# Kernel optimization log

Measured on AMD Instinct MI355X. Metric: run time of the kernel, lower is better.

The kernel has to match this reference:

```python
import jax, jax.numpy as jnp
import numpy as np

N_COMPANY = 16384
N_SECTOR = 64
PER_SECTOR = N_COMPANY // N_SECTOR  # 256, companies grouped contiguously by sector
WIN = 32
D_IN = 16
H_GRU = 64
H_INTRA = 64
H_INTER = 64
D_OUT = 4
E_INNER = 524288  # avg degree 32 within sectors


def setup_inputs() -> dict:
    key = jax.random.key(0)
    ks = jax.random.split(key, 20)
    s = 0.05

    daily_data_batch = jax.random.normal(ks[0], (WIN, N_COMPANY, D_IN), jnp.float32)

    rng = np.random.default_rng(0)
    dst = rng.integers(0, N_COMPANY, E_INNER)
    src = (dst // PER_SECTOR) * PER_SECTOR + rng.integers(0, PER_SECTOR, E_INNER)  # same-sector neighbors
    inner_edge = jnp.asarray(np.stack([src, dst]), jnp.int32)

    a, b = np.meshgrid(np.arange(N_SECTOR), np.arange(N_SECTOR), indexing="ij")
    oe = np.stack([a.ravel(), b.ravel()])
    oe = oe[:, oe[0] != oe[1]]  # fully-connected sector graph w/o self loops (GAT adds them)
    outer_edge = jnp.asarray(oe, jnp.int32)

    sector_ids = jnp.asarray(np.arange(N_COMPANY) // PER_SECTOR, jnp.int32)

    inp = {
        "daily_data_batch": daily_data_batch,
        "inner_edge": inner_edge,
        "outer_edge": outer_edge,
        "sector_ids": sector_ids,
        # BatchNorm1d(input_dim*window_size)
        "bn_gamma": jnp.ones((D_IN * WIN,), jnp.float32),
        "bn_beta": jnp.zeros((D_IN * WIN,), jnp.float32),
        # Graph GRU (per-node learnable initial hidden state)
        "gru_Wih": s * jax.random.normal(ks[1], (D_IN, 3 * H_GRU), jnp.float32),
        "gru_Whh": s * jax.random.normal(ks[2], (H_GRU, 3 * H_GRU), jnp.float32),
        "gru_bih": jnp.zeros((3 * H_GRU,), jnp.float32),
        "gru_bhh": jnp.zeros((3 * H_GRU,), jnp.float32),
        "gru_h0": s * jax.random.normal(ks[3], (N_COMPANY, H_GRU), jnp.float32),
        # intra-sector GATConv
        "gat1_W": s * jax.random.normal(ks[4], (H_GRU, H_INTRA), jnp.float32),
        "gat1_asrc": s * jax.random.normal(ks[5], (H_INTRA,), jnp.float32),
        "gat1_adst": s * jax.random.normal(ks[6], (H_INTRA,), jnp.float32),
        "gat1_b": jnp.zeros((H_INTRA,), jnp.float32),
        # inter-sector GATConv
        "gat2_W": s * jax.random.normal(ks[7], (H_INTRA, H_INTER), jnp.float32),
        "gat2_asrc": s * jax.random.normal(ks[8], (H_INTER,), jnp.float32),
        "gat2_adst": s * jax.random.normal(ks[9], (H_INTER,), jnp.float32),
        "gat2_b": jnp.zeros((H_INTER,), jnp.float32),
        # fusion / logit heads
        "fusion_W": s * jax.random.normal(ks[10], (H_GRU + H_INTRA + H_INTER, H_GRU), jnp.float32),
        "fusion_b": jnp.zeros((H_GRU,), jnp.float32),
        "logit_W": s * jax.random.normal(ks[11], (H_GRU, D_OUT), jnp.float32),
        "logit_b": jnp.zeros((D_OUT,), jnp.float32),
    }
    return inp


def _gat(x, edge, W, a_src, a_dst, b):
    """PyG-style single-head GATConv with default add_self_loops=True."""
    N = x.shape[0]
    h = x @ W  # [N, F]
    loops = jnp.arange(N, dtype=edge.dtype)
    src = jnp.concatenate([edge[0], loops])
    dst = jnp.concatenate([edge[1], loops])
    e = jax.nn.leaky_relu(h[src] @ a_src + h[dst] @ a_dst, 0.2)  # [E]
    # segment softmax over incoming edges per dst node
    m = jax.ops.segment_max(e, dst, num_segments=N)
    ex = jnp.exp(e - m[dst])
    denom = jax.ops.segment_sum(ex, dst, num_segments=N)
    alpha = ex / (denom[dst] + 1e-16)
    out = jax.ops.segment_sum(h[src] * alpha[:, None], dst, num_segments=N)
    return out + b


def _forward(daily_data_batch, inner_edge, outer_edge, sector_ids,
             bn_gamma, bn_beta,
             gru_Wih, gru_Whh, gru_bih, gru_bhh, gru_h0,
             gat1_W, gat1_asrc, gat1_adst, gat1_b,
             gat2_W, gat2_asrc, gat2_adst, gat2_b,
             fusion_W, fusion_b, logit_W, logit_b):
    W, N, D = daily_data_batch.shape
    # BatchNorm1d over companies (train-mode batch stats, eps=1e-5)
    xb = jnp.transpose(daily_data_batch, (1, 0, 2)).reshape(N, W * D)
    mu = xb.mean(axis=0)
    var = xb.var(axis=0)
    xb = (xb - mu) * jax.lax.rsqrt(var + 1e-5) * bn_gamma + bn_beta
    x = jnp.transpose(xb.reshape(N, W, D), (1, 0, 2))  # [W, N, D]

    # GRU over the window, per-node hidden state
    def step(h, xt):
        gi = xt @ gru_Wih + gru_bih
        gh = h @ gru_Whh + gru_bhh
        ir, iz, inn = jnp.split(gi, 3, axis=-1)
        hr, hz, hn = jnp.split(gh, 3, axis=-1)
        r = jax.nn.sigmoid(ir + hr)
        z = jax.nn.sigmoid(iz + hz)
        n = jnp.tanh(inn + r * hn)
        return (1.0 - z) * n + z * h, None

    seq_emb, _ = jax.lax.scan(step, gru_h0, x)  # [N, H_GRU]

    intra_emb = _gat(seq_emb, inner_edge, gat1_W, gat1_asrc, gat1_adst, gat1_b)  # [N, H_INTRA]

    # sector_separater + per-sector max pooling == segment_max
    sec_pool = jax.ops.segment_max(intra_emb, sector_ids, num_segments=N_SECTOR)  # [S, H_INTRA]
    sec_emb = _gat(sec_pool, outer_edge, gat2_W, gat2_asrc, gat2_adst, gat2_b)  # [S, H_INTER]
    sec_broad = sec_emb[sector_ids]  # repeat_interleave back to companies

    fusion_vec = jnp.concatenate([seq_emb, sec_broad, intra_emb], axis=-1)
    fusion_vec = jax.nn.relu(fusion_vec @ fusion_W + fusion_b)
    logits = jax.nn.softmax(fusion_vec @ logit_W + logit_b, axis=1)
    logits = jnp.cumsum(logits, axis=1)
    eps = 5e-08
    return jnp.clip(logits, eps, 1.0 - eps)


def reference(daily_data_batch, inner_edge, outer_edge, sector_ids,
              bn_gamma, bn_beta,
              gru_Wih, gru_Whh, gru_bih, gru_bhh, gru_h0,
              gat1_W, gat1_asrc, gat1_adst, gat1_b,
              gat2_W, gat2_asrc, gat2_adst, gat2_b,
              fusion_W, fusion_b, logit_W, logit_b):
    return _forward(daily_data_batch, inner_edge, outer_edge, sector_ids,
                    bn_gamma, bn_beta,
                    gru_Wih, gru_Whh, gru_bih, gru_bhh, gru_h0,
                    gat1_W, gat1_asrc, gat1_adst, gat1_b,
                    gat2_W, gat2_asrc, gat2_adst, gat2_b,
                    fusion_W, fusion_b, logit_W, logit_b)
```

## Files before the change

### kernel.cpp

```cpp
#include <hip/hip_runtime.h>

#define NC 16384
#define WIN 32
#define DI 16
#define EI 524288

typedef unsigned short u16;
typedef unsigned char u8;
typedef unsigned int u32;
typedef __attribute__((ext_vector_type(8))) short bfrag8;
typedef __attribute__((ext_vector_type(4))) float facc4;

__device__ __forceinline__ float bf2f(u16 u) { return __uint_as_float(((u32)u) << 16); }
__device__ __forceinline__ u16 f2bf(float f) {
    u32 u = __float_as_uint(f);
    u += 0x7FFFu + ((u >> 16) & 1u);
    return (u16)(u >> 16);
}
__device__ __forceinline__ float frcp(float x) { return __builtin_amdgcn_rcpf(x); }
__device__ __forceinline__ float ex2(float x) {
#if __has_builtin(__builtin_amdgcn_exp2f)
    return __builtin_amdgcn_exp2f(x);
#else
    return __expf(x * 0.69314718055994531f);
#endif
}
__device__ __forceinline__ u32 pk2bf(float a, float b) {
    u32 r;
    asm("v_cvt_pk_bf16_f32 %0, %1, %2" : "=v"(r) : "v"(a), "v"(b));
    return r;
}
__device__ __forceinline__ float lrelu(float x) { return x >= 0.0f ? x : 0.2f * x; }
__device__ __forceinline__ float loadf(const void* p, size_t i, bool f32) {
    return f32 ? ((const float*)p)[i] : bf2f(((const u16*)p)[i]);
}
__device__ __forceinline__ bool is_f32(const void* gamma) {
    return ((const u32*)gamma)[0] == 0x3F800000u;
}

#define O_WIMG  1024
#define O_BIMG  10240
#define O_BIH   16384
#define O_BHH   16576
#define O_G1W   16768
#define O_G1AS  20864
#define O_G1AD  20928
#define O_G1B   20992
#define O_G2W   21056
#define O_G2AS  25152
#define O_G2AD  25216
#define O_G2B   25280
#define O_FB    25344
#define O_LW    25408
#define O_LB    25664
#define O_FW16  25668
#define O_BNACC 31812
#define O_SEQ   40960
#define O_H1    1089536
#define O_INTRA 1613824
#define O_SPOOL 2138112
#define O_AS    2170880
#define O_AD    2187264
#define O_M     2203648

__global__ __launch_bounds__(256) void k_convert(const void* __restrict__ gamma,
                                                 const void* __restrict__ wih,
                                                 const void* __restrict__ whh,
                                                 const void* __restrict__ bih,
                                                 const void* __restrict__ bhh,
                                                 const void* __restrict__ g1w,
                                                 const void* __restrict__ g1as,
                                                 const void* __restrict__ g1ad,
                                                 const void* __restrict__ g1b,
                                                 const void* __restrict__ g2w,
                                                 const void* __restrict__ g2as,
                                                 const void* __restrict__ g2ad,
                                                 const void* __restrict__ g2b,
                                                 const void* __restrict__ fw,
                                                 const void* __restrict__ fb,
                                                 const void* __restrict__ lw,
                                                 const void* __restrict__ lb,
                                                 float* __restrict__ ws,
                                                 uint4* __restrict__ M16) {
    int gt = blockIdx.x * 256 + threadIdx.x;
    const int GS = 64 * 256;
    bool f32 = is_f32(gamma);
    const float KR = -1.4426950408889634f;
    const float KN = -2.8853900817779268f;
    u16* fw16 = (u16*)(ws + O_FW16);
    for (int i = gt; i < 12288; i += GS)
        fw16[i] = f32 ? f2bf(((const float*)fw)[i]) : ((const u16*)fw)[i];
    for (int i = gt; i < 4096; i += GS) {
        ws[O_G1W + i] = loadf(g1w, i, f32);
        ws[O_G2W + i] = loadf(g2w, i, f32);
    }
    if (gt < 64) {
        ws[O_G1AS + gt] = loadf(g1as, gt, f32);
        ws[O_G1AD + gt] = loadf(g1ad, gt, f32);
        ws[O_G1B + gt] = loadf(g1b, gt, f32);
        ws[O_G2AS + gt] = loadf(g2as, gt, f32);
        ws[O_G2AD + gt] = loadf(g2ad, gt, f32);
        ws[O_G2B + gt] = loadf(g2b, gt, f32);
        ws[O_FB + gt] = loadf(fb, gt, f32);
    }
    if (gt < 256) ws[O_LW + gt] = loadf(lw, gt, f32);
    if (gt < 4) ws[O_LB + gt] = loadf(lb, gt, f32);
    for (int i = gt; i < 1024; i += GS) ws[O_BNACC + i] = 0.f;
    const uint4 z4 = {0u, 0u, 0u, 0u};
    for (int i = gt; i < 262144; i += GS) M16[i] = z4;

    for (int i = gt; i < 9216; i += GS) {
        int trow = i / 36;
        int idx = i % 36;
        int w_ = trow >> 6, lane_ = trow & 63, li_ = lane_ & 15, q_ = lane_ >> 4;
        u16 lo, hi;
        if (idx < 24) {
            int g = idx >> 3, kc = (idx >> 2) & 1, j2 = idx & 3;
            float sc = (g < 2) ? KR : KN;
            int col = g * 64 + w_ * 16 + li_;
            int k = kc * 32 + q_ * 8 + j2 * 2;
            lo = f2bf(sc * loadf(whh, (size_t)k * 192 + col, f32));
            hi = f2bf(sc * loadf(whh, (size_t)(k + 1) * 192 + col, f32));
        } else {
            int idx2 = idx - 24;
            int g = idx2 >> 2, j2 = idx2 & 3;
            float sc = (g < 2) ? KR : KN;
            int col = g * 64 + w_ * 16 + li_;
            int k = q_ * 8 + j2 * 2;
            lo = (k < 16) ? f2bf(sc * loadf(wih, (size_t)k * 192 + col, f32)) : (u16)0;
            hi = (k + 1 < 16) ? f2bf(sc * loadf(wih, (size_t)(k + 1) * 192 + col, f32)) : (u16)0;
        }
        ((u32*)(ws + O_WIMG))[i] = (u32)lo | ((u32)hi << 16);
    }
    for (int i = gt; i < 1024; i += GS) {
        int trow = i >> 2, e = i & 3;
        int w_ = trow >> 6, lane_ = trow & 63, li_ = lane_ & 15;
        int c = w_ * 16 + li_;
        float v;
        if (e == 0) v = KR * (loadf(bih, c, f32) + loadf(bhh, c, f32));
        else if (e == 1) v = KR * (loadf(bih, 64 + c, f32) + loadf(bhh, 64 + c, f32));
        else if (e == 2) v = KN * loadf(bih, 128 + c, f32);
        else v = KN * loadf(bhh, 128 + c, f32);
        ws[O_BIMG + i] = v;
    }
}

__global__ __launch_bounds__(256) void k_prep(const void* __restrict__ daily,
                                              const void* __restrict__ gamma,
                                              float* __restrict__ bnacc,
                                              const int* __restrict__ edges,
                                              u32* __restrict__ M32) {
    __shared__ float rS[256 * 17];
    __shared__ float rQ[256 * 17];
    int bid = blockIdx.x;
    int tid = threadIdx.x;
    if (bid >= 128) {
        int g = (bid - 128) * 256 + tid;
        int4 s4 = ((const int4*)edges)[g];
        int4 d4 = ((const int4*)(edges + EI))[g];
        int ss[4] = {s4.x, s4.y, s4.z, s4.w};
        int dd[4] = {d4.x, d4.y, d4.z, d4.w};
#pragma unroll
        for (int i = 0; i < 4; i++) {
            int sl = ss[i] & 255;
            atomicAdd(&M32[dd[i] * 64 + (sl >> 2)], 1u << ((sl & 3) * 8));
        }
        return;
    }
    int w = bid >> 2, ch = bid & 3;
    bool f32 = is_f32(gamma);
    float s[16], q[16];
#pragma unroll
    for (int i = 0; i < 16; i++) { s[i] = 0.f; q[i] = 0.f; }
    for (int it = 0; it < 16; it++) {
        int c = ch * 4096 + it * 256 + tid;
        size_t base = ((size_t)w * NC + c) * DI;
        float v[16];
        if (f32) {
            const float4* p = (const float4*)((const float*)daily + base);
            float4 a = p[0], b = p[1], cc = p[2], d = p[3];
            v[0] = a.x; v[1] = a.y; v[2] = a.z; v[3] = a.w;
            v[4] = b.x; v[5] = b.y; v[6] = b.z; v[7] = b.w;
            v[8] = cc.x; v[9] = cc.y; v[10] = cc.z; v[11] = cc.w;
            v[12] = d.x; v[13] = d.y; v[14] = d.z; v[15] = d.w;
        } else {
            const uint4* p = (const uint4*)((const u16*)daily + base);
            uint4 a = p[0], b = p[1];
            u32 us[8] = {a.x, a.y, a.z, a.w, b.x, b.y, b.z, b.w};
#pragma unroll
            for (int i = 0; i < 8; i++) {
                v[2 * i] = __uint_as_float(us[i] << 16);
                v[2 * i + 1] = __uint_as_float(us[i] & 0xFFFF0000u);
            }
        }
#pragma unroll
        for (int i = 0; i < 16; i++) { s[i] += v[i]; q[i] += v[i] * v[i]; }
    }
#pragma unroll
    for (int i = 0; i < 16; i++) { rS[tid * 17 + i] = s[i]; rQ[tid * 17 + i] = q[i]; }
    __syncthreads();
    int f = tid & 15, g = tid >> 4;
    float ss = 0.f, qq = 0.f;
    for (int t = g * 16; t < g * 16 + 16; t++) { ss += rS[t * 17 + f]; qq += rQ[t * 17 + f]; }
    atomicAdd(&bnacc[w * 16 + f], ss);
    atomicAdd(&bnacc[512 + w * 16 + f], qq);
}

__global__ __launch_bounds__(256) void k_gru(const void* __restrict__ daily,
                                             const void* __restrict__ gamma,
                                             const void* __restrict__ beta,
                                             const void* __restrict__ h0_g,
                                             const float* __restrict__ ws,
                                             float* __restrict__ seq_out,
                                             u16* __restrict__ h1_out,
                                             float* __restrict__ asg,
                                             float* __restrict__ adg) {
    __shared__ __attribute__((aligned(16))) u16 sHd[2][16 * 72];
    __shared__ __attribute__((aligned(16))) u16 sXall[512 * 24];
    __shared__ float sSc[512], sSh[512];
    __shared__ float sRed[2][4][16];
    int tid = threadIdx.x;
    int w = tid >> 6, lane = tid & 63;
    int li = lane & 15, q = lane >> 4;
    int n0 = blockIdx.x * 16;
    int colw = w * 16 + li;
    bool f32 = is_f32(gamma);

    for (int f = tid; f < 512; f += 256) {
        float mu = ws[O_BNACC + f] * (1.0f / NC);
        float var = ws[O_BNACC + 512 + f] * (1.0f / NC) - mu * mu;
        float sc = loadf(gamma, f, f32) * rsqrtf(var + 1e-5f);
        sSc[f] = sc;
        sSh[f] = loadf(beta, f, f32) - mu * sc;
    }
    __syncthreads();

    for (int R = tid; R < 512; R += 256) {
        int t = R >> 4, m = R & 15;
        size_t base = ((size_t)t * NC + n0 + m) * DI;
        float xv[16];
        if (f32) {
            const float4* p = (const float4*)((const float*)daily + base);
            float4 a = p[0], b = p[1], c = p[2], d = p[3];
            xv[0] = a.x; xv[1] = a.y; xv[2] = a.z; xv[3] = a.w;
            xv[4] = b.x; xv[5] = b.y; xv[6] = b.z; xv[7] = b.w;
            xv[8] = c.x; xv[9] = c.y; xv[10] = c.z; xv[11] = c.w;
            xv[12] = d.x; xv[13] = d.y; xv[14] = d.z; xv[15] = d.w;
        } else {
            const uint4* p = (const uint4*)((const u16*)daily + base);
            uint4 a = p[0], b = p[1];
            u32 us[8] = {a.x, a.y, a.z, a.w, b.x, b.y, b.z, b.w};
#pragma unroll
            for (int i = 0; i < 8; i++) {
                xv[2 * i] = __uint_as_float(us[i] << 16);
                xv[2 * i + 1] = __uint_as_float(us[i] & 0xFFFF0000u);
            }
        }
        u32 pxu[8];
#pragma unroll
        for (int i = 0; i < 16; i += 2)
            pxu[i >> 1] = pk2bf(xv[i] * sSc[t * 16 + i] + sSh[t * 16 + i],
                                xv[i + 1] * sSc[t * 16 + i + 1] + sSh[t * 16 + i + 1]);
        *(uint4*)&sXall[R * 24] = *(const uint4*)&pxu[0];
        *(uint4*)&sXall[R * 24 + 8] = *(const uint4*)&pxu[4];
    }

    bfrag8 bh[3][2];
    bfrag8 bx[3];
    {
        const bfrag8* wf = (const bfrag8*)((const char*)(ws + O_WIMG) + (size_t)tid * 144);
        int c_ = 0;
#pragma unroll
        for (int g = 0; g < 3; g++)
#pragma unroll
            for (int kc = 0; kc < 2; kc++) bh[g][kc] = wf[c_++];
#pragma unroll
        for (int g = 0; g < 3; g++) bx[g] = wf[c_++];
    }
    float bR, bZ, bNX, bNH;
    {
        float4 b0 = ((const float4*)(ws + O_BIMG))[tid];
        bR = b0.x; bZ = b0.y; bNX = b0.z; bNH = b0.w;
    }

    float hC[4];
#pragma unroll
    for (int r = 0; r < 4; r++)
        hC[r] = loadf(h0_g, (size_t)(n0 + q * 4 + r) * 64 + colw, f32);
    {
        int hr = tid >> 4, hc = (tid & 15) * 4;
        u32 a = pk2bf(loadf(h0_g, (size_t)(n0 + hr) * 64 + hc, f32),
                      loadf(h0_g, (size_t)(n0 + hr) * 64 + hc + 1, f32));
        u32 b = pk2bf(loadf(h0_g, (size_t)(n0 + hr) * 64 + hc + 2, f32),
                      loadf(h0_g, (size_t)(n0 + hr) * 64 + hc + 3, f32));
        uint2 v2; v2.x = a; v2.y = b;
        *(uint2*)&sHd[0][hr * 72 + hc] = v2;
    }
    __syncthreads();

    bfrag8 ax = (bfrag8){0, 0, 0, 0, 0, 0, 0, 0};
    if (q < 2) ax = *(const bfrag8*)&sXall[li * 24 + q * 8];
    for (int t = 0; t < WIN; t++) {
        int p = t & 1;
        bfrag8 ah0 = *(const bfrag8*)&sHd[p][li * 72 + q * 8];
        bfrag8 ah1 = *(const bfrag8*)&sHd[p][li * 72 + 32 + q * 8];
        int tn = (t + 1) & (WIN - 1);
        bfrag8 axn = (bfrag8){0, 0, 0, 0, 0, 0, 0, 0};
        if (q < 2) axn = *(const bfrag8*)&sXall[(tn * 16 + li) * 24 + q * 8];
        facc4 aR = __builtin_amdgcn_mfma_f32_16x16x32_bf16(ax, bx[0], (facc4){bR, bR, bR, bR}, 0, 0, 0);
        facc4 aZ = __builtin_amdgcn_mfma_f32_16x16x32_bf16(ax, bx[1], (facc4){bZ, bZ, bZ, bZ}, 0, 0, 0);
        facc4 aNX = __builtin_amdgcn_mfma_f32_16x16x32_bf16(ax, bx[2], (facc4){bNX, bNX, bNX, bNX}, 0, 0, 0);
        facc4 aNH = __builtin_amdgcn_mfma_f32_16x16x32_bf16(ah0, bh[2][0], (facc4){bNH, bNH, bNH, bNH}, 0, 0, 0);
        aR = __builtin_amdgcn_mfma_f32_16x16x32_bf16(ah0, bh[0][0], aR, 0, 0, 0);
        aZ = __builtin_amdgcn_mfma_f32_16x16x32_bf16(ah0, bh[1][0], aZ, 0, 0, 0);
        aNH = __builtin_amdgcn_mfma_f32_16x16x32_bf16(ah1, bh[2][1], aNH, 0, 0, 0);
        aR = __builtin_amdgcn_mfma_f32_16x16x32_bf16(ah1, bh[0][1], aR, 0, 0, 0);
        aZ = __builtin_amdgcn_mfma_f32_16x16x32_bf16(ah1, bh[1][1], aZ, 0, 0, 0);
#pragma unroll
        for (int r = 0; r < 4; r++) {
            float gr = frcp(1.0f + ex2(aR[r]));
            float gz = frcp(1.0f + ex2(aZ[r]));
            float narg = aNX[r] + gr * aNH[r];
            float gn = 2.0f * frcp(1.0f + ex2(narg)) - 1.0f;
            hC[r] = gn + gz * (hC[r] - gn);
        }
#pragma unroll
        for (int rp = 0; rp < 4; rp += 2) {
            u32 pk = pk2bf(hC[rp], hC[rp + 1]);
            sHd[p ^ 1][(q * 4 + rp) * 72 + colw] = (u16)pk;
            sHd[p ^ 1][(q * 4 + rp + 1) * 72 + colw] = (u16)(pk >> 16);
        }
        __syncthreads();
        ax = axn;
    }

#pragma unroll
    for (int r = 0; r < 4; r++)
        seq_out[(size_t)(n0 + q * 4 + r) * 64 + colw] = hC[r];

    bfrag8 a0 = *(const bfrag8*)&sHd[0][li * 72 + q * 8];
    bfrag8 a1 = *(const bfrag8*)&sHd[0][li * 72 + 32 + q * 8];
    const facc4 zf = {0.f, 0.f, 0.f, 0.f};
    bfrag8 bg0, bg1;
#pragma unroll
    for (int j = 0; j < 8; j++) {
        bg0[j] = (short)f2bf(ws[O_G1W + (q * 8 + j) * 64 + colw]);
        bg1[j] = (short)f2bf(ws[O_G1W + (32 + q * 8 + j) * 64 + colw]);
    }
    facc4 acc = __builtin_amdgcn_mfma_f32_16x16x32_bf16(a0, bg0, zf, 0, 0, 0);
    acc = __builtin_amdgcn_mfma_f32_16x16x32_bf16(a1, bg1, acc, 0, 0, 0);
    float a1s_j = ws[O_G1AS + colw], a1d_j = ws[O_G1AD + colw];
    float pAs[4], pAd[4];
#pragma unroll
    for (int r = 0; r < 4; r++) {
        h1_out[(size_t)(n0 + q * 4 + r) * 64 + colw] = f2bf(acc[r]);
        pAs[r] = acc[r] * a1s_j;
        pAd[r] = acc[r] * a1d_j;
    }
#pragma unroll
    for (int o = 1; o < 16; o <<= 1)
#pragma unroll
        for (int r = 0; r < 4; r++) {
            pAs[r] += __shfl_xor(pAs[r], o);
            pAd[r] += __shfl_xor(pAd[r], o);
        }
    if (li == 0) {
#pragma unroll
        for (int r = 0; r < 4; r++) {
            sRed[0][w][q * 4 + r] = pAs[r];
            sRed[1][w][q * 4 + r] = pAd[r];
        }
    }
    __syncthreads();
    if (tid < 16) {
        asg[n0 + tid] = sRed[0][0][tid] + sRed[0][1][tid] + sRed[0][2][tid] + sRed[0][3][tid];
        adg[n0 + tid] = sRed[1][0][tid] + sRed[1][1][tid] + sRed[1][2][tid] + sRed[1][3][tid];
    }
}

__global__ __launch_bounds__(256) void k_gat1agg(const u16* __restrict__ h1g,
                                                 const float* __restrict__ ws,
                                                 const u8* __restrict__ M8,
                                                 const float* __restrict__ asg,
                                                 const float* __restrict__ adg,
                                                 u16* __restrict__ intra,
                                                 float* __restrict__ spool8) {
    __shared__ __attribute__((aligned(16))) u16 hT[64 * 264];
    __shared__ __attribute__((aligned(16))) u16 sP[32 * 264];
    __shared__ float sAs[256], sAd[32], sB[64], sRS[32];
    __shared__ float sRSp[8][32];
    __shared__ float wmax[4];
    int tid = threadIdx.x;
    int sector = blockIdx.x >> 3;
    int dstbase = sector * 256 + (blockIdx.x & 7) * 32;
    int sbase = sector * 256;
    {
#pragma unroll
        for (int p = 0; p < 8; p++) {
            int row = p * 32 + (tid >> 3);
            int c0 = (tid & 7) * 8;
            uint4 v = *(const uint4*)(h1g + (size_t)(sbase + row) * 64 + c0);
            u16 e[8];
            *(uint4*)e = v;
#pragma unroll
            for (int i = 0; i < 8; i++) hT[(c0 + i) * 264 + row] = e[i];
        }
    }
    sAs[tid] = asg[sbase + tid];
    if (tid < 32) sAd[tid] = adg[dstbase + tid];
    if (tid < 64) sB[tid] = ws[O_G1B + tid];
    __syncthreads();
    int lane = tid & 63, w = tid >> 6;
    int li = lane & 15, q = lane >> 4;
    {
        float a = sAs[tid];
#pragma unroll
        for (int o = 1; o < 64; o <<= 1) a = fmaxf(a, __shfl_xor(a, o));
        if (lane == 0) wmax[w] = a;
    }
    __syncthreads();
    float maxA = fmaxf(fmaxf(wmax[0], wmax[1]), fmaxf(wmax[2], wmax[3]));

    int prow = tid >> 3, pcg = tid & 7;
    {
        float adr_p = sAd[prow];
        float mrow_p = lrelu(maxA + adr_p);
        float lsum = 0.f;
        const u8* mp = M8 + (size_t)(dstbase + prow) * 256 + pcg * 32;
        uint4 mva = *(const uint4*)mp;
        uint4 mvb = *(const uint4*)(mp + 16);
        u32 wsrc[8] = {mva.x, mva.y, mva.z, mva.w, mvb.x, mvb.y, mvb.z, mvb.w};
#pragma unroll
        for (int i2 = 0; i2 < 16; i2++) {
            int i0 = 2 * i2;
            u32 mb0 = (wsrc[i0 >> 2] >> ((i0 & 3) * 8)) & 255u;
            u32 mb1 = (wsrc[i0 >> 2] >> (((i0 + 1) & 3) * 8)) & 255u;
            int c = pcg * 32 + i0;
            float e0 = lrelu(sAs[c] + adr_p);
            float e1 = lrelu(sAs[c + 1] + adr_p);
            float v0 = (float)mb0 * __expf(e0 - mrow_p);
            float v1 = (float)mb1 * __expf(e1 - mrow_p);
            u16 b0 = f2bf(v0), b1 = f2bf(v1);
            *(u32*)&sP[prow * 264 + pcg * 32 + i0] = (u32)b0 | ((u32)b1 << 16);
            lsum += bf2f(b0) + bf2f(b1);
        }
        sRSp[pcg][prow] = lsum;
    }
    __syncthreads();

    facc4 acc[2];
    acc[0] = (facc4){0.f, 0.f, 0.f, 0.f};
    acc[1] = (facc4){0.f, 0.f, 0.f, 0.f};
#pragma unroll
    for (int kc = 0; kc < 8; kc++) {
        bfrag8 bfh = *(const bfrag8*)&hT[(w * 16 + li) * 264 + kc * 32 + q * 8];
#pragma unroll
        for (int mt = 0; mt < 2; mt++) {
            bfrag8 af = *(const bfrag8*)&sP[(mt * 16 + li) * 264 + kc * 32 + q * 8];
            acc[mt] = __builtin_amdgcn_mfma_f32_16x16x32_bf16(af, bfh, acc[mt], 0, 0, 0);
        }
    }
    if (tid < 32) {
        float s = 0.f;
#pragma unroll
        for (int g = 0; g < 8; g++) s += sRSp[g][tid];
        sRS[tid] = s;
    }
    __syncthreads();

    float vmax = -1e30f;
    int colL = w * 16 + li;
#pragma unroll
    for (int mt = 0; mt < 2; mt++) {
#pragma unroll
        for (int r = 0; r < 4; r++) {
            int row = mt * 16 + q * 4 + r;
            int d = dstbase + row;
            int selfI = (blockIdx.x & 7) * 32 + row;
            float adr = sAd[row];
            float es = lrelu(sAs[selfI] + adr);
            float mrow = lrelu(maxA + adr);
            float exS = __expf(es - mrow);
            float denom = sRS[row] + exS;
            float inv = frcp(denom + 1e-16f);
            float selfh = bf2f(hT[colL * 264 + selfI]);
            float val = (acc[mt][r] + exS * selfh) * inv + sB[colL];
            intra[(size_t)d * 64 + colL] = f2bf(val);
            vmax = fmaxf(vmax, val);
        }
    }
    vmax = fmaxf(vmax, __shfl_xor(vmax, 16));
    vmax = fmaxf(vmax, __shfl_xor(vmax, 32));
    if (q == 0) spool8[(size_t)blockIdx.x * 64 + colL] = vmax;
}

__global__ __launch_bounds__(256) void k_fusion(const float* __restrict__ seq,
                                                const float* __restrict__ spool8,
                                                const u16* __restrict__ intra,
                                                const float* __restrict__ ws,
                                                const void* __restrict__ gamma,
                                                void* __restrict__ out) {
    __shared__ __attribute__((aligned(16))) union {
        struct { u16 sPmax[64 * 72]; float sH2[64 * 68]; } p0;
        struct { u16 sV[64 * 200]; float sFus[64 * 68]; } p1;
    } U;
    __shared__ float sSemb[64], sAs2[64], sAd2[64];
    __shared__ float sFB[64], sLW[256], sLB[4];
    __shared__ float red2[512];
    int tid = threadIdx.x, n0 = blockIdx.x * 64;
    int sid = blockIdx.x >> 2;
    bool f32 = is_f32(gamma);
    int lane = tid & 63, w = tid >> 6;
    int li = lane & 15, q = lane >> 4;
    int colw = w * 16 + li;

    for (int i = tid; i < 4096; i += 256) {
        int n = i >> 6, k = i & 63;
        const float* pp = &spool8[(size_t)(n * 8) * 64 + k];
        float m = pp[0];
#pragma unroll
        for (int p = 1; p < 8; p++) m = fmaxf(m, pp[p * 64]);
        U.p0.sPmax[n * 72 + k] = f2bf(m);
    }
    bfrag8 bw2[2];
#pragma unroll
    for (int kc = 0; kc < 2; kc++)
#pragma unroll
        for (int j = 0; j < 8; j++)
            bw2[kc][j] = (short)f2bf(ws[O_G2W + (kc * 32 + q * 8 + j) * 64 + colw]);
    __syncthreads();
    {
        const facc4 zf = {0.f, 0.f, 0.f, 0.f};
#pragma unroll
        for (int mt = 0; mt < 4; mt++) {
            bfrag8 af0 = *(const bfrag8*)&U.p0.sPmax[(mt * 16 + li) * 72 + q * 8];
            bfrag8 af1 = *(const bfrag8*)&U.p0.sPmax[(mt * 16 + li) * 72 + 32 + q * 8];
            facc4 a2 = __builtin_amdgcn_mfma_f32_16x16x32_bf16(af0, bw2[0], zf, 0, 0, 0);
            a2 = __builtin_amdgcn_mfma_f32_16x16x32_bf16(af1, bw2[1], a2, 0, 0, 0);
#pragma unroll
            for (int r = 0; r < 4; r++)
                U.p0.sH2[(mt * 16 + q * 4 + r) * 68 + colw] = a2[r];
        }
    }
    __syncthreads();
    {
        int n = tid >> 2, jg = tid & 3, j0 = jg * 16;
        float ps = 0.f, pd = 0.f;
#pragma unroll
        for (int i = 0; i < 16; i++) {
            float v = U.p0.sH2[n * 68 + j0 + i];
            ps += v * ws[O_G2AS + j0 + i];
            pd += v * ws[O_G2AD + j0 + i];
        }
        red2[(n * 4 + jg) * 2] = ps;
        red2[(n * 4 + jg) * 2 + 1] = pd;
    }
    __syncthreads();
    if (tid < 64) {
        float s = 0.f, dd = 0.f;
        for (int g = 0; g < 4; g++) { s += red2[(tid * 4 + g) * 2]; dd += red2[(tid * 4 + g) * 2 + 1]; }
        sAs2[tid] = s; sAd2[tid] = dd;
    }
    __syncthreads();
    if (tid < 64) {
        float e = lrelu(sAs2[tid] + sAd2[sid]);
        float m = e;
        for (int o = 32; o; o >>= 1) m = fmaxf(m, __shfl_xor(m, o));
        float ex = __expf(e - m);
        float den = ex;
        for (int o = 32; o; o >>= 1) den += __shfl_xor(den, o);
        float inv = frcp(den + 1e-16f);
        float o_ = 0.f;
        for (int l = 0; l < 64; l++) {
            float a = __shfl(ex, l);
            o_ += a * U.p0.sH2[l * 68 + tid];
        }
        sSemb[tid] = o_ * inv + ws[O_G2B + tid];
    }
    if (tid < 64) sFB[tid] = ws[O_FB + tid];
    sLW[tid] = ws[O_LW + tid];
    if (tid < 4) sLB[tid] = ws[O_LB + tid];
    __syncthreads();

    {
        int c = tid >> 2, p = tid & 3;
        u16 px[16];
        const float* rp = seq + (size_t)(n0 + c) * 64 + p * 16;
#pragma unroll
        for (int i = 0; i < 16; i += 4) {
            float4 v = *(const float4*)&rp[i];
            px[i] = f2bf(v.x); px[i + 1] = f2bf(v.y); px[i + 2] = f2bf(v.z); px[i + 3] = f2bf(v.w);
        }
        *(uint4*)&U.p1.sV[c * 200 + p * 16] = *(const uint4*)&px[0];
        *(uint4*)&U.p1.sV[c * 200 + p * 16 + 8] = *(const uint4*)&px[8];
#pragma unroll
        for (int i = 0; i < 16; i++) px[i] = f2bf(sSemb[p * 16 + i]);
        *(uint4*)&U.p1.sV[c * 200 + 64 + p * 16] = *(const uint4*)&px[0];
        *(uint4*)&U.p1.sV[c * 200 + 64 + p * 16 + 8] = *(const uint4*)&px[8];
        const u16* ip = intra + (size_t)(n0 + c) * 64 + p * 16;
        *(uint4*)&U.p1.sV[c * 200 + 128 + p * 16] = *(const uint4*)ip;
        *(uint4*)&U.p1.sV[c * 200 + 128 + p * 16 + 8] = *(const uint4*)(ip + 8);
    }
    const u16* fw16g = (const u16*)(ws + O_FW16);
    bfrag8 bwf[6];
#pragma unroll
    for (int kc = 0; kc < 6; kc++)
#pragma unroll
        for (int j = 0; j < 8; j++)
            bwf[kc][j] = (short)fw16g[(kc * 32 + q * 8 + j) * 64 + colw];
    __syncthreads();

    facc4 acc[4];
#pragma unroll
    for (int mt = 0; mt < 4; mt++) acc[mt] = (facc4){0.f, 0.f, 0.f, 0.f};
#pragma unroll
    for (int kc = 0; kc < 6; kc++) {
#pragma unroll
        for (int mt = 0; mt < 4; mt++) {
            bfrag8 av = *(const bfrag8*)&U.p1.sV[(mt * 16 + li) * 200 + kc * 32 + q * 8];
            acc[mt] = __builtin_amdgcn_mfma_f32_16x16x32_bf16(av, bwf[kc], acc[mt], 0, 0, 0);
        }
    }
    float fb = sFB[colw];
#pragma unroll
    for (int mt = 0; mt < 4; mt++)
#pragma unroll
        for (int r = 0; r < 4; r++) {
            float v = fmaxf(acc[mt][r] + fb, 0.f);
            U.p1.sFus[(mt * 16 + q * 4 + r) * 68 + colw] = v;
        }
    __syncthreads();

    if (tid < 64) {
        float l[4] = {sLB[0], sLB[1], sLB[2], sLB[3]};
        for (int j = 0; j < 64; j++) {
            float v = U.p1.sFus[tid * 68 + j];
            l[0] += v * sLW[j * 4 + 0];
            l[1] += v * sLW[j * 4 + 1];
            l[2] += v * sLW[j * 4 + 2];
            l[3] += v * sLW[j * 4 + 3];
        }
        float m = fmaxf(fmaxf(l[0], l[1]), fmaxf(l[2], l[3]));
        float e0 = __expf(l[0] - m), e1 = __expf(l[1] - m), e2 = __expf(l[2] - m), e3 = __expf(l[3] - m);
        float is = frcp(e0 + e1 + e2 + e3);
        float c0 = e0 * is;
        float c1 = c0 + e1 * is;
        float c2 = c1 + e2 * is;
        float c3 = c2 + e3 * is;
        const float lo = 5e-8f, hi = 1.0f - 5e-8f;
        c0 = fminf(fmaxf(c0, lo), hi);
        c1 = fminf(fmaxf(c1, lo), hi);
        c2 = fminf(fmaxf(c2, lo), hi);
        c3 = fminf(fmaxf(c3, lo), hi);
        size_t ob = (size_t)(n0 + tid) * 4;
        if (f32) {
            *(float4*)&((float*)out)[ob] = make_float4(c0, c1, c2, c3);
        } else {
            *(ushort4*)&((u16*)out)[ob] = make_ushort4(f2bf(c0), f2bf(c1), f2bf(c2), f2bf(c3));
        }
    }
}

extern "C" void kernel_launch(void* const* d_in, const int* in_sizes, int n_in,
                              void* d_out, int out_size, void* d_ws, size_t ws_size,
                              hipStream_t stream) {
    const void* daily = d_in[0];
    const int* inner = (const int*)d_in[1];
    const void* gamma = d_in[4];
    const void* beta = d_in[5];
    const void* wih = d_in[6];
    const void* whh = d_in[7];
    const void* bih = d_in[8];
    const void* bhh = d_in[9];
    const void* h0 = d_in[10];
    const void* g1w = d_in[11];
    const void* g1as = d_in[12];
    const void* g1ad = d_in[13];
    const void* g1b = d_in[14];
    const void* g2w = d_in[15];
    const void* g2as = d_in[16];
    const void* g2ad = d_in[17];
    const void* g2b = d_in[18];
    const void* fw = d_in[19];
    const void* fb = d_in[20];
    const void* lw = d_in[21];
    const void* lb = d_in[22];

    float* ws = (float*)d_ws;
    u16* h1g = (u16*)(ws + O_H1);
    u16* intra = (u16*)(ws + O_INTRA);
    u8* M8 = (u8*)(ws + O_M);

    k_convert<<<64, 256, 0, stream>>>(gamma, wih, whh, bih, bhh, g1w, g1as, g1ad, g1b,
                                      g2w, g2as, g2ad, g2b, fw, fb, lw, lb, ws, (uint4*)M8);
    k_prep<<<640, 256, 0, stream>>>(daily, gamma, ws + O_BNACC, inner, (u32*)M8);
    k_gru<<<1024, 256, 0, stream>>>(daily, gamma, beta, h0, ws, ws + O_SEQ, h1g, ws + O_AS, ws + O_AD);
    k_gat1agg<<<512, 256, 0, stream>>>(h1g, ws, M8, ws + O_AS, ws + O_AD, intra, ws + O_SPOOL);
    k_fusion<<<256, 256, 0, stream>>>(ws + O_SEQ, ws + O_SPOOL, intra, ws, gamma, d_out);
}
```

Measured before the change: 212.7 us.

## Split sector GAT into single-block kernel and parallelize fusion logits head

The sector-level GAT (pooling, projection, attention) was previously recomputed redundantly in each of the 256 fusion blocks. It now runs once in a new single-block kernel that writes all 64 sector embeddings into the workspace, reusing the spool buffer. The fusion kernel just loads its sector's embedding. The final logit/softmax/cumsum stage now uses all 256 threads (four per company, with shuffles) instead of 64. The cost is an extra kernel launch and a serial one-block kernel on the critical path.

```diff
diff --git a/kernel.cpp b/kernel.cpp
--- a/kernel.cpp
+++ b/kernel.cpp
@@ -494,25 +494,16 @@
     if (q == 0) spool8[(size_t)blockIdx.x * 64 + colL] = vmax;
 }
 
-__global__ __launch_bounds__(256) void k_fusion(const float* __restrict__ seq,
-                                                const float* __restrict__ spool8,
-                                                const u16* __restrict__ intra,
-                                                const float* __restrict__ ws,
-                                                const void* __restrict__ gamma,
-                                                void* __restrict__ out) {
-    __shared__ __attribute__((aligned(16))) union {
-        struct { u16 sPmax[64 * 72]; float sH2[64 * 68]; } p0;
-        struct { u16 sV[64 * 200]; float sFus[64 * 68]; } p1;
-    } U;
-    __shared__ float sSemb[64], sAs2[64], sAd2[64];
-    __shared__ float sFB[64], sLW[256], sLB[4];
+__global__ __launch_bounds__(256) void k_gat2(float* __restrict__ ws) {
+    __shared__ __attribute__((aligned(16))) u16 sPmax[64 * 72];
+    __shared__ float sH2[64 * 68];
+    __shared__ float sAs2[64], sAd2[64];
     __shared__ float red2[512];
-    int tid = threadIdx.x, n0 = blockIdx.x * 64;
-    int sid = blockIdx.x >> 2;
-    bool f32 = is_f32(gamma);
+    int tid = threadIdx.x;
     int lane = tid & 63, w = tid >> 6;
     int li = lane & 15, q = lane >> 4;
     int colw = w * 16 + li;
+    const float* spool8 = ws + O_SPOOL;
 
     for (int i = tid; i < 4096; i += 256) {
         int n = i >> 6, k = i & 63;
@@ -520,7 +511,7 @@
         float m = pp[0];
 #pragma unroll
         for (int p = 1; p < 8; p++) m = fmaxf(m, pp[p * 64]);
-        U.p0.sPmax[n * 72 + k] = f2bf(m);
+        sPmax[n * 72 + k] = f2bf(m);
     }
     bfrag8 bw2[2];
 #pragma unroll
@@ -533,13 +524,13 @@
         const facc4 zf = {0.f, 0.f, 0.f, 0.f};
 #pragma unroll
         for (int mt = 0; mt < 4; mt++) {
-            bfrag8 af0 = *(const bfrag8*)&U.p0.sPmax[(mt * 16 + li) * 72 + q * 8];
-            bfrag8 af1 = *(const bfrag8*)&U.p0.sPmax[(mt * 16 + li) * 72 + 32 + q * 8];
+            bfrag8 af0 = *(const bfrag8*)&sPmax[(mt * 16 + li) * 72 + q * 8];
+            bfrag8 af1 = *(const bfrag8*)&sPmax[(mt * 16 + li) * 72 + 32 + q * 8];
             facc4 a2 = __builtin_amdgcn_mfma_f32_16x16x32_bf16(af0, bw2[0], zf, 0, 0, 0);
             a2 = __builtin_amdgcn_mfma_f32_16x16x32_bf16(af1, bw2[1], a2, 0, 0, 0);
 #pragma unroll
             for (int r = 0; r < 4; r++)
-                U.p0.sH2[(mt * 16 + q * 4 + r) * 68 + colw] = a2[r];
+                sH2[(mt * 16 + q * 4 + r) * 68 + colw] = a2[r];
         }
     }
     __syncthreads();
@@ -548,7 +539,7 @@
         float ps = 0.f, pd = 0.f;
 #pragma unroll
         for (int i = 0; i < 16; i++) {
-            float v = U.p0.sH2[n * 68 + j0 + i];
+            float v = sH2[n * 68 + j0 + i];
             ps += v * ws[O_G2AS + j0 + i];
             pd += v * ws[O_G2AD + j0 + i];
         }
@@ -562,8 +553,12 @@
         sAs2[tid] = s; sAd2[tid] = dd;
     }
     __syncthreads();
-    if (tid < 64) {
-        float e = lrelu(sAs2[tid] + sAd2[sid]);
+    float as_l = sAs2[lane];
+    float* semb = ws + O_SPOOL;
+    float g2b_l = ws[O_G2B + lane];
+    for (int d0 = 0; d0 < 16; d0++) {
+        int dst = w * 16 + d0;
+        float e = lrelu(as_l + sAd2[dst]);
         float m = e;
         for (int o = 32; o; o >>= 1) m = fmaxf(m, __shfl_xor(m, o));
         float ex = __expf(e - m);
@@ -573,11 +568,32 @@
         float o_ = 0.f;
         for (int l = 0; l < 64; l++) {
             float a = __shfl(ex, l);
-            o_ += a * U.p0.sH2[l * 68 + tid];
-        }
-        sSemb[tid] = o_ * inv + ws[O_G2B + tid];
-    }
-    if (tid < 64) sFB[tid] = ws[O_FB + tid];
+            o_ += a * sH2[l * 68 + lane];
+        }
+        semb[dst * 64 + lane] = o_ * inv + g2b_l;
+    }
+}
+
+__global__ __launch_bounds__(256) void k_fusion(const float* __restrict__ seq,
+                                                const float* __restrict__ semb,
+                                                const u16* __restrict__ intra,
+                                                const float* __restrict__ ws,
+                                                const void* __restrict__ gamma,
+                                                void* __restrict__ out) {
+    __shared__ __attribute__((aligned(16))) u16 sV[64 * 200];
+    __shared__ float sFus[64 * 68];
+    __shared__ float sSemb[64], sFB[64], sLW[256], sLB[4];
+    int tid = threadIdx.x, n0 = blockIdx.x * 64;
+    int sid = blockIdx.x >> 2;
+    bool f32 = is_f32(gamma);
+    int lane = tid & 63, w = tid >> 6;
+    int li = lane & 15, q = lane >> 4;
+    int colw = w * 16 + li;
+
+    if (tid < 64) {
+        sSemb[tid] = semb[(size_t)sid * 64 + tid];
+        sFB[tid] = ws[O_FB + tid];
+    }
     sLW[tid] = ws[O_LW + tid];
     if (tid < 4) sLB[tid] = ws[O_LB + tid];
     __syncthreads();
@@ -591,15 +607,15 @@
             float4 v = *(const float4*)&rp[i];
             px[i] = f2bf(v.x); px[i + 1] = f2bf(v.y); px[i + 2] = f2bf(v.z); px[i + 3] = f2bf(v.w);
         }
-        *(uint4*)&U.p1.sV[c * 200 + p * 16] = *(const uint4*)&px[0];
-        *(uint4*)&U.p1.sV[c * 200 + p * 16 + 8] = *(const uint4*)&px[8];
+        *(uint4*)&sV[c * 200 + p * 16] = *(const uint4*)&px[0];
+        *(uint4*)&sV[c * 200 + p * 16 + 8] = *(const uint4*)&px[8];
 #pragma unroll
         for (int i = 0; i < 16; i++) px[i] = f2bf(sSemb[p * 16 + i]);
-        *(uint4*)&U.p1.sV[c * 200 + 64 + p * 16] = *(const uint4*)&px[0];
-        *(uint4*)&U.p1.sV[c * 200 + 64 + p * 16 + 8] = *(const uint4*)&px[8];
+        *(uint4*)&sV[c * 200 + 64 + p * 16] = *(const uint4*)&px[0];
+        *(uint4*)&sV[c * 200 + 64 + p * 16 + 8] = *(const uint4*)&px[8];
         const u16* ip = intra + (size_t)(n0 + c) * 64 + p * 16;
-        *(uint4*)&U.p1.sV[c * 200 + 128 + p * 16] = *(const uint4*)ip;
-        *(uint4*)&U.p1.sV[c * 200 + 128 + p * 16 + 8] = *(const uint4*)(ip + 8);
+        *(uint4*)&sV[c * 200 + 128 + p * 16] = *(const uint4*)ip;
+        *(uint4*)&sV[c * 200 + 128 + p * 16 + 8] = *(const uint4*)(ip + 8);
     }
     const u16* fw16g = (const u16*)(ws + O_FW16);
     bfrag8 bwf[6];
@@ -617,7 +633,7 @@
     for (int kc = 0; kc < 6; kc++) {
 #pragma unroll
         for (int mt = 0; mt < 4; mt++) {
-            bfrag8 av = *(const bfrag8*)&U.p1.sV[(mt * 16 + li) * 200 + kc * 32 + q * 8];
+            bfrag8 av = *(const bfrag8*)&sV[(mt * 16 + li) * 200 + kc * 32 + q * 8];
             acc[mt] = __builtin_amdgcn_mfma_f32_16x16x32_bf16(av, bwf[kc], acc[mt], 0, 0, 0);
         }
     }
@@ -627,37 +643,31 @@
 #pragma unroll
         for (int r = 0; r < 4; r++) {
             float v = fmaxf(acc[mt][r] + fb, 0.f);
-            U.p1.sFus[(mt * 16 + q * 4 + r) * 68 + colw] = v;
-        }
-    __syncthreads();
-
-    if (tid < 64) {
-        float l[4] = {sLB[0], sLB[1], sLB[2], sLB[3]};
-        for (int j = 0; j < 64; j++) {
-            float v = U.p1.sFus[tid * 68 + j];
-            l[0] += v * sLW[j * 4 + 0];
-            l[1] += v * sLW[j * 4 + 1];
-            l[2] += v * sLW[j * 4 + 2];
-            l[3] += v * sLW[j * 4 + 3];
-        }
-        float m = fmaxf(fmaxf(l[0], l[1]), fmaxf(l[2], l[3]));
-        float e0 = __expf(l[0] - m), e1 = __expf(l[1] - m), e2 = __expf(l[2] - m), e3 = __expf(l[3] - m);
-        float is = frcp(e0 + e1 + e2 + e3);
-        float c0 = e0 * is;
-        float c1 = c0 + e1 * is;
-        float c2 = c1 + e2 * is;
-        float c3 = c2 + e3 * is;
+            sFus[(mt * 16 + q * 4 + r) * 68 + colw] = v;
+        }
+    __syncthreads();
+
+    {
+        int cpy = tid >> 2, cls = tid & 3;
+        float lv = sLB[cls];
+        for (int j = 0; j < 64; j++) lv += sFus[cpy * 68 + j] * sLW[j * 4 + cls];
+        float m2 = fmaxf(lv, __shfl_xor(lv, 1));
+        m2 = fmaxf(m2, __shfl_xor(m2, 2));
+        float e = __expf(lv - m2);
+        float s2 = e + __shfl_xor(e, 1);
+        s2 += __shfl_xor(s2, 2);
+        float is = frcp(s2);
+        float pref = e;
+        float t1 = __shfl_up(pref, 1);
+        if (cls >= 1) pref += t1;
+        float t2 = __shfl_up(pref, 2);
+        if (cls >= 2) pref += t2;
+        float ck = pref * is;
         const float lo = 5e-8f, hi = 1.0f - 5e-8f;
-        c0 = fminf(fmaxf(c0, lo), hi);
-        c1 = fminf(fmaxf(c1, lo), hi);
-        c2 = fminf(fmaxf(c2, lo), hi);
-        c3 = fminf(fmaxf(c3, lo), hi);
-        size_t ob = (size_t)(n0 + tid) * 4;
-        if (f32) {
-            *(float4*)&((float*)out)[ob] = make_float4(c0, c1, c2, c3);
-        } else {
-            *(ushort4*)&((u16*)out)[ob] = make_ushort4(f2bf(c0), f2bf(c1), f2bf(c2), f2bf(c3));
-        }
+        ck = fminf(fmaxf(ck, lo), hi);
+        size_t ob = (size_t)(n0 + cpy) * 4 + cls;
+        if (f32) ((float*)out)[ob] = ck;
+        else ((u16*)out)[ob] = f2bf(ck);
     }
 }
 
@@ -696,5 +706,6 @@
     k_prep<<<640, 256, 0, stream>>>(daily, gamma, ws + O_BNACC, inner, (u32*)M8);
     k_gru<<<1024, 256, 0, stream>>>(daily, gamma, beta, h0, ws, ws + O_SEQ, h1g, ws + O_AS, ws + O_AD);
     k_gat1agg<<<512, 256, 0, stream>>>(h1g, ws, M8, ws + O_AS, ws + O_AD, intra, ws + O_SPOOL);
+    k_gat2<<<1, 256, 0, stream>>>(ws);
     k_fusion<<<256, 256, 0, stream>>>(ws + O_SEQ, ws + O_SPOOL, intra, ws, gamma, d_out);
 }
```

Measured after the change: 235.6 us. 10.8% more time.
